# Optimization experiments

Hardware: AMD Instinct MI355X
Metric: run time of the kernel (lower is better)

## Reference

```python
import jax, jax.numpy as jnp
import numpy as np

NUM_HEADS = 4
ALPHA = 0.2  # LeakyReLU negative slope


def setup_inputs() -> dict:
    key = jax.random.key(0)
    k1, k2 = jax.random.split(key)
    input_tensor = jax.random.normal(k1, (2, 4096, 128), dtype=jnp.float32)
    adj_matrix = jax.random.randint(k2, (4096, 4096), 0, 2, dtype=jnp.int32)
    return {"input_tensor": input_tensor, "adj_matrix": adj_matrix}


def reference(input_tensor, adj_matrix):
    B, S, F = input_tensor.shape
    H = NUM_HEADS
    x = input_tensor.reshape(B, S, H, F // H)          # (B,S,H,K)
    # full dense score matrix, QK^T-like with shared projection (identity)
    scores = jnp.einsum('bihk,bjhk->bhij', x, x)        # (B,H,S,S)
    scores = jax.nn.leaky_relu(scores, negative_slope=ALPHA)
    # adjacency mask broadcast over (B,H)
    scores = jnp.where(adj_matrix[None, None, :, :] == 0, -jnp.inf, scores)
    probs = jax.nn.softmax(scores, axis=-1)             # dropout p=0 -> identity
    out = jnp.einsum('bhij,bjhk->bihk', probs, x)       # (B,S,H,K)
    return out.reshape(B, S, F)                          # concat=True
```

## Files before the change

### kernel.cpp

```cpp
#include <hip/hip_runtime.h>
#include <stdint.h>

#define SEQ 4096
#define FDIM 128
#define NH 4
#define HD 32
#define NB 2
#define NROWS (NB * NH * SEQ)
#define LOG2E 1.4426950408889634f
#define KVB 128
#define VCS 136
#define VPHALF (32 * VCS)

typedef float f32x4 __attribute__((ext_vector_type(4)));
typedef __bf16 bf16x8 __attribute__((ext_vector_type(8)));

__device__ __forceinline__ unsigned short f2bf(float f) {
  unsigned int u = __builtin_bit_cast(unsigned int, f);
  return (unsigned short)((u + 0x7FFFu + ((u >> 16) & 1u)) >> 16);
}

__global__ void cvt_kernel(const float* __restrict__ in, unsigned short* __restrict__ out) {
  int i = (blockIdx.x * 256 + threadIdx.x) * 4;
  float4 v = *reinterpret_cast<const float4*>(in + i);
  ushort4 o;
  o.x = f2bf(v.x); o.y = f2bf(v.y); o.z = f2bf(v.z); o.w = f2bf(v.w);
  *reinterpret_cast<ushort4*>(out + i) = o;
}

__global__ void adjpack_kernel(const int* __restrict__ adj, unsigned short* __restrict__ bits16) {
  size_t t = (size_t)blockIdx.x * 256 + threadIdx.x;
  const uint4* p = reinterpret_cast<const uint4*>(adj) + t * 4;
  uint4 a = p[0], b = p[1], c = p[2], d = p[3];
  unsigned m = 0;
  m |= (a.x != 0) ? 1u : 0u;        m |= (a.y != 0) ? 2u : 0u;
  m |= (a.z != 0) ? 4u : 0u;        m |= (a.w != 0) ? 8u : 0u;
  m |= (b.x != 0) ? 16u : 0u;       m |= (b.y != 0) ? 32u : 0u;
  m |= (b.z != 0) ? 64u : 0u;       m |= (b.w != 0) ? 128u : 0u;
  m |= (c.x != 0) ? 256u : 0u;      m |= (c.y != 0) ? 512u : 0u;
  m |= (c.z != 0) ? 1024u : 0u;     m |= (c.w != 0) ? 2048u : 0u;
  m |= (d.x != 0) ? 4096u : 0u;     m |= (d.y != 0) ? 8192u : 0u;
  m |= (d.z != 0) ? 16384u : 0u;    m |= (d.w != 0) ? 32768u : 0u;
  bits16[t] = (unsigned short)m;
}

#define STEP(T, RB, WBUF)                                                       \
  {                                                                             \
    __syncthreads();                                                            \
    const bool pfok = (T) + 1 < NT;                                             \
    if (pfok) {      \
      kptr += KVB * FDIM;                                                       \
      k0 = *reinterpret_cast<const uint4*>(kptr);                               \
      k1 = *reinterpret_cast<const uint4*>(kptr + 64 * FDIM);                   \
      sptr += KVB * FDIM;                                                       \
      r0 = *reinterpret_cast<const uint2*>(sptr);                               \
      r1 = *reinterpret_cast<const uint2*>(sptr + FDIM);                        \
      r2 = *reinterpret_cast<const uint2*>(sptr + 64 * FDIM);                   \
      r3 = *reinterpret_cast<const uint2*>(sptr + 65 * FDIM);                   \
      wnv = *reinterpret_cast<const uint4*>(&brow[bcol0 + 2 * ((T) + 1)]);      \
    }                                                                           \
    _Pragma("unroll") for (int hf = 0; hf < 2; ++hf) {                          \
      f32x4 sc[4];                                                              \
      __builtin_amdgcn_s_setprio(1);                                            \
      _Pragma("unroll") for (int t4 = 0; t4 < 4; ++t4) {                        \
        bf16x8 kf = __builtin_bit_cast(bf16x8,                                  \
            *reinterpret_cast<const uint4*>(                                    \
                &Kl[RB][hf * 64 + t4 * 16 + ql][g * 8]));                       \
        sc[t4] = __builtin_amdgcn_mfma_f32_16x16x32_bf16(kf, qf, zf, 0, 0, 0);  \
      }                                                                         \
      __builtin_amdgcn_s_setprio(0);                                            \
      const unsigned long long wsh = (hf ? wc1 : wc0) >> (4 * g);               \
      const int mwl = (int)(unsigned)wsh, mwh = (int)(unsigned)(wsh >> 32);     \
      float pf4[4][4];                                                          \
      _Pragma("unroll") for (int t4 = 0; t4 < 4; ++t4) {                        \
        const int word = (t4 & 2) ? mwh : mwl;                                  \
        _Pragma("unroll") for (int r = 0; r < 4; ++r) {                         \
          float v = sc[t4][r];                                                  \
          v = fmaxf(v, 0.2f * v);                               \
          float e = __builtin_amdgcn_exp2f(v);              \
          const int msk = __builtin_amdgcn_sbfe(word, 16 * (t4 & 1) + r, 1);    \
          pf4[t4][r] = __builtin_bit_cast(                                      \
              float, __builtin_bit_cast(unsigned, e) & (unsigned)msk);          \
        }                                                                       \
      }                                                                         \
      __builtin_amdgcn_s_setprio(1);                                            \
      _Pragma("unroll") for (int uu = 0; uu < 2; ++uu) {                        \
        const int u = 2 * hf + uu;                                              \
        bf16x8 pa;                                                              \
        _Pragma("unroll") for (int tp = 0; tp < 2; ++tp)                        \
            _Pragma("unroll") for (int r = 0; r < 4; ++r)                       \
                pa[tp * 4 + r] = (__bf16)pf4[2 * uu + tp][r];                   \
        bf16x8 vf0 = __builtin_bit_cast(bf16x8,                                 \
            *reinterpret_cast<const uint4*>(&Vp[RB][ql * VCS + u * 32 + g * 8]));        \
        bf16x8 vf1 = __builtin_bit_cast(bf16x8,                                 \
            *reinterpret_cast<const uint4*>(&Vp[RB][(16 + ql) * VCS + u * 32 + g * 8])); \
        acc0 = __builtin_amdgcn_mfma_f32_16x16x32_bf16(pa, vf0, acc0, 0, 0, 0); \
        acc1 = __builtin_amdgcn_mfma_f32_16x16x32_bf16(pa, vf1, acc1, 0, 0, 0); \
        accL = __builtin_amdgcn_mfma_f32_16x16x32_bf16(pa, ones, accL, 0, 0, 0);\
      }                                                                         \
      __builtin_amdgcn_s_setprio(0);                                            \
    }                                                                           \
    if (pfok) {   \
      *reinterpret_cast<uint4*>(&Kl[WBUF][krow][kq * 8]) = k0;                  \
      *reinterpret_cast<uint4*>(&Kl[WBUF][64 + krow][kq * 8]) = k1;             \
      unsigned* vw = reinterpret_cast<unsigned*>(&Vp[WBUF][0]) + pi0h;          \
      vw[(4 * c4 + 0) * 68] = __builtin_amdgcn_perm(r1.x, r0.x, selA);          \
      vw[(4 * c4 + 1) * 68] = __builtin_amdgcn_perm(r1.x, r0.x, selB);          \
      vw[(4 * c4 + 2) * 68] = __builtin_amdgcn_perm(r1.y, r0.y, selA);          \
      vw[(4 * c4 + 3) * 68] = __builtin_amdgcn_perm(r1.y, r0.y, selB);          \
      vw[(4 * c4 + 0) * 68 + 32] = __builtin_amdgcn_perm(r3.x, r2.x, selA);     \
      vw[(4 * c4 + 1) * 68 + 32] = __builtin_amdgcn_perm(r3.x, r2.x, selB);     \
      vw[(4 * c4 + 2) * 68 + 32] = __builtin_amdgcn_perm(r3.y, r2.y, selA);     \
      vw[(4 * c4 + 3) * 68 + 32] = __builtin_amdgcn_perm(r3.y, r2.y, selB);     \
    }                                                                           \
    wc0 = (unsigned long long)wnv.x | ((unsigned long long)wnv.y << 32);        \
    wc1 = (unsigned long long)wnv.z | ((unsigned long long)wnv.w << 32);        \
  }

template <int NSPLIT>
__global__ __launch_bounds__(256, 4) void gat_kernel(
    const unsigned short* __restrict__ xbf,
    const unsigned long long* __restrict__ bits,
    float* __restrict__ dst,
    float* __restrict__ lbuf) {
  __shared__ __align__(16) unsigned short Kl[2][KVB][40];
  __shared__ __align__(16) unsigned short Vp[2][VPHALF];

  const int bh = blockIdx.y;
  const int b = bh >> 2;
  const int h = bh & 3;
  const int tid = threadIdx.x;
  const int wid = tid >> 6;
  const int lane = tid & 63;
  const int g = lane >> 4;
  const int ql = lane & 15;
  const int qw = blockIdx.x * 64 + wid * 16;
  const int jbase = blockIdx.z * (SEQ / NSPLIT);
  const int NT = (SEQ / NSPLIT) / KVB;

  const unsigned short* xb = xbf + ((size_t)b * SEQ) * FDIM + h * HD;

  bf16x8 qraw = __builtin_bit_cast(bf16x8,
      *reinterpret_cast<const uint4*>(xb + (size_t)(qw + ql) * FDIM + g * 8));
  bf16x8 qf;
#pragma unroll
  for (int e = 0; e < 8; ++e) qf[e] = (__bf16)((float)qraw[e] * LOG2E);

  bf16x8 ones;
#pragma unroll
  for (int e = 0; e < 8; ++e) ones[e] = (__bf16)1.0f;
  const f32x4 zf = {0.f, 0.f, 0.f, 0.f};

  f32x4 acc0 = {0.f, 0.f, 0.f, 0.f};
  f32x4 acc1 = {0.f, 0.f, 0.f, 0.f};
  f32x4 accL = {0.f, 0.f, 0.f, 0.f};

  const unsigned long long* brow = bits + (size_t)(qw + ql) * (SEQ / 64);
  const int bcol0 = jbase >> 6;

  const int krow = tid >> 2;
  const int kq = tid & 3;
  const unsigned short* kptr = xb + (size_t)(jbase + krow) * FDIM + kq * 8;

  const int s3 = (tid >> 3) & 7;
  const int pr = (s3 & 1) | (((s3 >> 1) & 1) << 1) | ((wid & 1) << 2) |
                 (((s3 >> 2) & 1) << 3) | ((wid >> 1) << 4);
  const int c4 = tid & 7;
  const unsigned short* sptr = xb + (size_t)(jbase + 2 * pr) * FDIM + c4 * 4;

  const int pi0h = 16 * (pr >> 4) + 4 * ((pr >> 1) & 3) + 2 * ((pr >> 3) & 1) + (pr & 1);

  const unsigned selA = 0x05040100u;
  const unsigned selB = 0x07060302u;

  uint4 k0 = *reinterpret_cast<const uint4*>(kptr);
  uint4 k1 = *reinterpret_cast<const uint4*>(kptr + 64 * FDIM);
  uint2 r0 = *reinterpret_cast<const uint2*>(sptr);
  uint2 r1 = *reinterpret_cast<const uint2*>(sptr + FDIM);
  uint2 r2 = *reinterpret_cast<const uint2*>(sptr + 64 * FDIM);
  uint2 r3 = *reinterpret_cast<const uint2*>(sptr + 65 * FDIM);
  uint4 wnv = *reinterpret_cast<const uint4*>(&brow[bcol0]);
  unsigned long long wc0 = (unsigned long long)wnv.x | ((unsigned long long)wnv.y << 32);
  unsigned long long wc1 = (unsigned long long)wnv.z | ((unsigned long long)wnv.w << 32);
  *reinterpret_cast<uint4*>(&Kl[0][krow][kq * 8]) = k0;
  *reinterpret_cast<uint4*>(&Kl[0][64 + krow][kq * 8]) = k1;
  {
    unsigned* vw = reinterpret_cast<unsigned*>(&Vp[0][0]) + pi0h;
    vw[(4 * c4 + 0) * 68] = __builtin_amdgcn_perm(r1.x, r0.x, selA);
    vw[(4 * c4 + 1) * 68] = __builtin_amdgcn_perm(r1.x, r0.x, selB);
    vw[(4 * c4 + 2) * 68] = __builtin_amdgcn_perm(r1.y, r0.y, selA);
    vw[(4 * c4 + 3) * 68] = __builtin_amdgcn_perm(r1.y, r0.y, selB);
    vw[(4 * c4 + 0) * 68 + 32] = __builtin_amdgcn_perm(r3.x, r2.x, selA);
    vw[(4 * c4 + 1) * 68 + 32] = __builtin_amdgcn_perm(r3.x, r2.x, selB);
    vw[(4 * c4 + 2) * 68 + 32] = __builtin_amdgcn_perm(r3.y, r2.y, selA);
    vw[(4 * c4 + 3) * 68 + 32] = __builtin_amdgcn_perm(r3.y, r2.y, selB);
  }

  for (int t = 0; t < NT; t += 2) {
    STEP(t, 0, 1);
    STEP(t + 1, 1, 0);
  }

  if (NSPLIT == 1) {
#pragma unroll
    for (int r = 0; r < 4; ++r) {
      const float inv = 1.f / accL[r];
      const size_t o = ((size_t)b * SEQ + (size_t)(qw + 4 * g + r)) * FDIM + h * HD;
      dst[o + ql] = acc0[r] * inv;
      dst[o + 16 + ql] = acc1[r] * inv;
    }
  } else {
    float* Op = dst + (((size_t)blockIdx.z * (NB * NH) + bh) * SEQ) * HD;
#pragma unroll
    for (int r = 0; r < 4; ++r) {
      const int q = qw + 4 * g + r;
      Op[(size_t)q * HD + ql] = acc0[r];
      Op[(size_t)q * HD + 16 + ql] = acc1[r];
    }
    if (ql == 0) {
#pragma unroll
      for (int r = 0; r < 4; ++r)
        lbuf[(size_t)blockIdx.z * NROWS + (size_t)bh * SEQ + qw + 4 * g + r] = accL[r];
    }
  }
}

template <int NSPLIT>
__global__ __launch_bounds__(256) void combine_kernel(
    const float* __restrict__ Op, const float* __restrict__ lbuf, float* __restrict__ out) {
  const int idx = blockIdx.x * 256 + threadIdx.x;
  const int row = idx >> 3;
  const int dc = (idx & 7) * 4;
  float lt = 0.f;
  float4 o = {0.f, 0.f, 0.f, 0.f};
#pragma unroll
  for (int s = 0; s < NSPLIT; ++s) {
    lt += lbuf[(size_t)s * NROWS + row];
    float4 v = *reinterpret_cast<const float4*>(Op + ((size_t)s * NROWS + row) * HD + dc);
    o.x += v.x; o.y += v.y; o.z += v.z; o.w += v.w;
  }
  const float inv = 1.f / lt;
  const int bh = row >> 12;
  const int q = row & (SEQ - 1);
  const int b = bh >> 2;
  const int h = bh & 3;
  float4 w;
  w.x = o.x * inv; w.y = o.y * inv; w.z = o.z * inv; w.w = o.w * inv;
  *reinterpret_cast<float4*>(out + ((size_t)b * SEQ + q) * FDIM + h * HD + dc) = w;
}

extern "C" void kernel_launch(void* const* d_in, const int* in_sizes, int n_in,
                              void* d_out, int out_size, void* d_ws, size_t ws_size,
                              hipStream_t stream) {
  (void)in_sizes; (void)n_in; (void)out_size;
  const float* x = (const float*)d_in[0];
  const int* adj = (const int*)d_in[1];
  float* outp = (float*)d_out;

  unsigned short* xbf = (unsigned short*)d_ws;
  unsigned short* bits16 = (unsigned short*)((char*)d_ws + (2u << 20));
  float* Opart = (float*)((char*)d_ws + (4u << 20));
  auto need = [](int s) {
    return (size_t)(4u << 20) + (size_t)s * NROWS * HD * 4 + (size_t)s * NROWS * 4;
  };

  cvt_kernel<<<(NB * SEQ * FDIM) / (256 * 4), 256, 0, stream>>>(x, xbf);
  adjpack_kernel<<<(SEQ * SEQ) / (16 * 256), 256, 0, stream>>>(adj, bits16);

  const unsigned long long* bits = (const unsigned long long*)bits16;
  if (ws_size >= need(4)) {
    float* mlb = (float*)((char*)d_ws + (4u << 20) + (size_t)4 * NROWS * HD * 4);
    dim3 grid(SEQ / 64, NB * NH, 4);
    gat_kernel<4><<<grid, 256, 0, stream>>>(xbf, bits, Opart, mlb);
    combine_kernel<4><<<(NROWS * 8) / 256, 256, 0, stream>>>(Opart, mlb, outp);
  } else if (ws_size >= need(2)) {
    float* mlb = (float*)((char*)d_ws + (4u << 20) + (size_t)2 * NROWS * HD * 4);
    dim3 grid(SEQ / 64, NB * NH, 2);
    gat_kernel<2><<<grid, 256, 0, stream>>>(xbf, bits, Opart, mlb);
    combine_kernel<2><<<(NROWS * 8) / 256, 256, 0, stream>>>(Opart, mlb, outp);
  } else {
    dim3 grid(SEQ / 64, NB * NH, 1);
    gat_kernel<1><<<grid, 256, 0, stream>>>(xbf, bits, outp, nullptr);
  }
}
```

Baseline: 73.17 us.

## Double query tile per block to 128 rows with 512 threads sharing K/V tiles

```diff
diff --git a/kernel.cpp b/kernel.cpp
--- a/kernel.cpp
+++ b/kernel.cpp
@@ -9,6 +9,7 @@
 #define NROWS (NB * NH * SEQ)
 #define LOG2E 1.4426950408889634f
 #define KVB 128
+#define QB 128
 #define VCS 136
 #define VPHALF (32 * VCS)
 
@@ -51,12 +52,9 @@
     if (pfok) {      \
       kptr += KVB * FDIM;                                                       \
       k0 = *reinterpret_cast<const uint4*>(kptr);                               \
-      k1 = *reinterpret_cast<const uint4*>(kptr + 64 * FDIM);                   \
       sptr += KVB * FDIM;                                                       \
       r0 = *reinterpret_cast<const uint2*>(sptr);                               \
       r1 = *reinterpret_cast<const uint2*>(sptr + FDIM);                        \
-      r2 = *reinterpret_cast<const uint2*>(sptr + 64 * FDIM);                   \
-      r3 = *reinterpret_cast<const uint2*>(sptr + 65 * FDIM);                   \
       wnv = *reinterpret_cast<const uint4*>(&brow[bcol0 + 2 * ((T) + 1)]);      \
     }                                                                           \
     _Pragma("unroll") for (int hf = 0; hf < 2; ++hf) {                          \
@@ -102,23 +100,18 @@
     }                                                                           \
     if (pfok) {   \
       *reinterpret_cast<uint4*>(&Kl[WBUF][krow][kq * 8]) = k0;                  \
-      *reinterpret_cast<uint4*>(&Kl[WBUF][64 + krow][kq * 8]) = k1;             \
       unsigned* vw = reinterpret_cast<unsigned*>(&Vp[WBUF][0]) + pi0h;          \
       vw[(4 * c4 + 0) * 68] = __builtin_amdgcn_perm(r1.x, r0.x, selA);          \
       vw[(4 * c4 + 1) * 68] = __builtin_amdgcn_perm(r1.x, r0.x, selB);          \
       vw[(4 * c4 + 2) * 68] = __builtin_amdgcn_perm(r1.y, r0.y, selA);          \
       vw[(4 * c4 + 3) * 68] = __builtin_amdgcn_perm(r1.y, r0.y, selB);          \
-      vw[(4 * c4 + 0) * 68 + 32] = __builtin_amdgcn_perm(r3.x, r2.x, selA);     \
-      vw[(4 * c4 + 1) * 68 + 32] = __builtin_amdgcn_perm(r3.x, r2.x, selB);     \
-      vw[(4 * c4 + 2) * 68 + 32] = __builtin_amdgcn_perm(r3.y, r2.y, selA);     \
-      vw[(4 * c4 + 3) * 68 + 32] = __builtin_amdgcn_perm(r3.y, r2.y, selB);     \
     }                                                                           \
     wc0 = (unsigned long long)wnv.x | ((unsigned long long)wnv.y << 32);        \
     wc1 = (unsigned long long)wnv.z | ((unsigned long long)wnv.w << 32);        \
   }
 
 template <int NSPLIT>
-__global__ __launch_bounds__(256, 4) void gat_kernel(
+__global__ __launch_bounds__(512, 8) void gat_kernel(
     const unsigned short* __restrict__ xbf,
     const unsigned long long* __restrict__ bits,
     float* __restrict__ dst,
@@ -134,7 +127,7 @@
   const int lane = tid & 63;
   const int g = lane >> 4;
   const int ql = lane & 15;
-  const int qw = blockIdx.x * 64 + wid * 16;
+  const int qw = blockIdx.x * QB + wid * 16;
   const int jbase = blockIdx.z * (SEQ / NSPLIT);
   const int NT = (SEQ / NSPLIT) / KVB;
 
@@ -162,38 +155,29 @@
   const int kq = tid & 3;
   const unsigned short* kptr = xb + (size_t)(jbase + krow) * FDIM + kq * 8;
 
-  const int s3 = (tid >> 3) & 7;
-  const int pr = (s3 & 1) | (((s3 >> 1) & 1) << 1) | ((wid & 1) << 2) |
-                 (((s3 >> 2) & 1) << 3) | ((wid >> 1) << 4);
+  const int pr = tid >> 3;
   const int c4 = tid & 7;
   const unsigned short* sptr = xb + (size_t)(jbase + 2 * pr) * FDIM + c4 * 4;
 
-  const int pi0h = 16 * (pr >> 4) + 4 * ((pr >> 1) & 3) + 2 * ((pr >> 3) & 1) + (pr & 1);
+  const int pi0h = 32 * (pr >> 5) + 16 * ((pr >> 4) & 1) + 4 * ((pr >> 1) & 3) +
+                   2 * ((pr >> 3) & 1) + (pr & 1);
 
   const unsigned selA = 0x05040100u;
   const unsigned selB = 0x07060302u;
 
   uint4 k0 = *reinterpret_cast<const uint4*>(kptr);
-  uint4 k1 = *reinterpret_cast<const uint4*>(kptr + 64 * FDIM);
   uint2 r0 = *reinterpret_cast<const uint2*>(sptr);
   uint2 r1 = *reinterpret_cast<const uint2*>(sptr + FDIM);
-  uint2 r2 = *reinterpret_cast<const uint2*>(sptr + 64 * FDIM);
-  uint2 r3 = *reinterpret_cast<const uint2*>(sptr + 65 * FDIM);
   uint4 wnv = *reinterpret_cast<const uint4*>(&brow[bcol0]);
   unsigned long long wc0 = (unsigned long long)wnv.x | ((unsigned long long)wnv.y << 32);
   unsigned long long wc1 = (unsigned long long)wnv.z | ((unsigned long long)wnv.w << 32);
   *reinterpret_cast<uint4*>(&Kl[0][krow][kq * 8]) = k0;
-  *reinterpret_cast<uint4*>(&Kl[0][64 + krow][kq * 8]) = k1;
   {
     unsigned* vw = reinterpret_cast<unsigned*>(&Vp[0][0]) + pi0h;
     vw[(4 * c4 + 0) * 68] = __builtin_amdgcn_perm(r1.x, r0.x, selA);
     vw[(4 * c4 + 1) * 68] = __builtin_amdgcn_perm(r1.x, r0.x, selB);
     vw[(4 * c4 + 2) * 68] = __builtin_amdgcn_perm(r1.y, r0.y, selA);
     vw[(4 * c4 + 3) * 68] = __builtin_amdgcn_perm(r1.y, r0.y, selB);
-    vw[(4 * c4 + 0) * 68 + 32] = __builtin_amdgcn_perm(r3.x, r2.x, selA);
-    vw[(4 * c4 + 1) * 68 + 32] = __builtin_amdgcn_perm(r3.x, r2.x, selB);
-    vw[(4 * c4 + 2) * 68 + 32] = __builtin_amdgcn_perm(r3.y, r2.y, selA);
-    vw[(4 * c4 + 3) * 68 + 32] = __builtin_amdgcn_perm(r3.y, r2.y, selB);
   }
 
   for (int t = 0; t < NT; t += 2) {
@@ -270,16 +254,16 @@
   const unsigned long long* bits = (const unsigned long long*)bits16;
   if (ws_size >= need(4)) {
     float* mlb = (float*)((char*)d_ws + (4u << 20) + (size_t)4 * NROWS * HD * 4);
-    dim3 grid(SEQ / 64, NB * NH, 4);
-    gat_kernel<4><<<grid, 256, 0, stream>>>(xbf, bits, Opart, mlb);
+    dim3 grid(SEQ / QB, NB * NH, 4);
+    gat_kernel<4><<<grid, 512, 0, stream>>>(xbf, bits, Opart, mlb);
     combine_kernel<4><<<(NROWS * 8) / 256, 256, 0, stream>>>(Opart, mlb, outp);
   } else if (ws_size >= need(2)) {
     float* mlb = (float*)((char*)d_ws + (4u << 20) + (size_t)2 * NROWS * HD * 4);
-    dim3 grid(SEQ / 64, NB * NH, 2);
-    gat_kernel<2><<<grid, 256, 0, stream>>>(xbf, bits, Opart, mlb);
+    dim3 grid(SEQ / QB, NB * NH, 2);
+    gat_kernel<2><<<grid, 512, 0, stream>>>(xbf, bits, Opart, mlb);
     combine_kernel<2><<<(NROWS * 8) / 256, 256, 0, stream>>>(Opart, mlb, outp);
   } else {
-    dim3 grid(SEQ / 64, NB * NH, 1);
-    gat_kernel<1><<<grid, 256, 0, stream>>>(xbf, bits, outp, nullptr);
-  }
-}
+    dim3 grid(SEQ / QB, NB * NH, 1);
+    gat_kernel<1><<<grid, 512, 0, stream>>>(xbf, bits, outp, nullptr);
+  }
+}
```

After: 74.48 us. No clear change (+1.8%).
